# Kernel tuning notes

Measured on AMD Instinct MI355X. Metric: run time of the kernel, lower is better.

Reference implementation:

```python
import jax, jax.numpy as jnp
import numpy as np

# Module hyperparameters (init_kwargs)
OSFREQ = 8.0
MAXFREQ = 1.0
SP = 1.0
THRESH = 0.0

B, C, T = 8, 64, 1200


def _periodogram_cfg(n_samples):
    # Mirrors hypercoil's _periodogram_cfg
    timespan = SP * (n_samples + 1) - 1
    all_samples = np.arange(SP, timespan + 1, SP)
    freqstep = 1.0 / (timespan * OSFREQ)
    angular_frequencies = 2.0 * np.pi * np.arange(
        freqstep, MAXFREQ * n_samples / (2.0 * timespan) + freqstep, freqstep
    )
    return (
        jnp.asarray(angular_frequencies, jnp.float32),  # [K]
        jnp.asarray(all_samples, jnp.float32),          # [T]
    )


def setup_inputs() -> dict:
    key = jax.random.key(0)
    k1, k2 = jax.random.split(key)
    data = jax.random.normal(k1, (B, C, T), dtype=jnp.float32)
    mask = jax.random.randint(k2, (B, T), 0, 2).astype(bool)
    return {"input": data, "mask": mask}


def _fit_spectrum(basis, m, dm):
    # basis: [B,K,T] shifted trig basis; m: [B,T] mask weights; dm: [B,C,T] masked data
    num = jnp.einsum('bkt,bct->bkc', basis, dm)              # masked projection
    denom = jnp.einsum('bkt,bkt,bt->bk', basis, basis, m)    # masked basis norm
    coef = num / denom[..., None]
    if THRESH > 0:
        a = jnp.abs(coef)
        coef = jnp.where(a / a.max() > THRESH, coef, 0.0)
    return coef


def spectral_interpolate(data, mask):
    omega, t = _periodogram_cfg(data.shape[-1])  # [K], [T]
    m = mask.astype(data.dtype)                  # [B,T]
    arg2 = 2.0 * omega[:, None] * t[None, :]     # [K,T]
    # Lomb-Scargle time offsets tau per (batch, frequency), over observed samples only
    tau = jnp.arctan2(
        jnp.einsum('bt,kt->bk', m, jnp.sin(arg2)),
        jnp.einsum('bt,kt->bk', m, jnp.cos(arg2)),
    ) / (2.0 * omega)[None, :]                   # [B,K]
    theta = omega[None, :, None] * (t[None, None, :] - tau[:, :, None])  # [B,K,T]
    cosb = jnp.cos(theta)
    sinb = jnp.sin(theta)
    dm = data * m[:, None, :]                    # masked (degraded) data [B,C,T]
    c_coef = _fit_spectrum(cosb, m, dm)          # [B,K,C]
    s_coef = _fit_spectrum(sinb, m, dm)
    recon = (jnp.einsum('bkt,bkc->bct', cosb, c_coef)
             + jnp.einsum('bkt,bkc->bct', sinb, s_coef))      # [B,C,T]
    # Normalise: match std of reconstruction to std of observed data
    std_recon = jnp.std(recon, axis=-1, ddof=1, keepdims=True)
    cnt = m.sum(-1)[:, None, None]
    mu = dm.sum(-1, keepdims=True) / cnt
    var = ((data - mu) ** 2 * m[:, None, :]).sum(-1, keepdims=True) / (cnt - 1.0)
    std_orig = jnp.sqrt(var)
    recon = recon * (std_orig / std_recon)
    # Keep observed samples; fill censored samples with reconstruction
    return jnp.where(mask[:, None, :], data, recon)


def reference(input, mask):
    return spectral_interpolate(input, mask)
```

## Files before the change

### kernel.cpp

```cpp
#include <hip/hip_runtime.h>
#include <math.h>

#define B_ 8
#define C_ 64
#define M_ 512
#define T_ 1200
#define TP2 1280
#define KP 4864
#define K2P 9728
#define SPLITK 8
#define KCH 1216
#define NST1 20
#define NST2 19
#define TCH 152

#ifndef M_PI
#define M_PI 3.14159265358979323846
#endif

typedef _Float16 h8 __attribute__((ext_vector_type(8)));
typedef float f32x16 __attribute__((ext_vector_type(16)));
union H8 { h8 h; float4 v; _Float16 e[8]; };
union HP { _Float16 hh[2]; unsigned u; };
union F4U { float4 v; float f[4]; };

#define Z16v {0.f,0.f,0.f,0.f,0.f,0.f,0.f,0.f,0.f,0.f,0.f,0.f,0.f,0.f,0.f,0.f}
#define MFMA32(a, b, c) __builtin_amdgcn_mfma_f32_32x32x16_f16(a, b, c, 0, 0, 0)

__device__ __forceinline__ float2 cmul(float2 a, float2 b) {
    return make_float2(a.x * b.x - a.y * b.y, a.y * b.x + a.x * b.y);
}

__device__ __forceinline__ void gload16(const void* g, void* l) {
    __builtin_amdgcn_global_load_lds(
        (const __attribute__((address_space(1))) unsigned int*)g,
        (__attribute__((address_space(3))) unsigned int*)l, 16, 0, 0);
}

__device__ int detect_mode(const void* mask_raw) {
    __shared__ int sb0, sb1;
    if (threadIdx.x == 0) { sb0 = 0; sb1 = 0; }
    __syncthreads();
    const unsigned* wi = (const unsigned*)mask_raw;
    const float* wf = (const float*)mask_raw;
    int nw = (B_ * T_) >> 2;
    int badI = 0, badF = 0;
    for (int i = threadIdx.x; i < nw; i += blockDim.x) {
        unsigned v = wi[i];
        badI |= (v > 1u);
        float f = wf[i];
        badF |= !(f == 0.0f || f == 1.0f);
    }
    if (badI) sb0 = 1;
    if (badF) sb1 = 1;
    __syncthreads();
    return (!sb0) ? 0 : ((!sb1) ? 1 : 2);
}

__device__ __forceinline__ float mval(const void* mask_raw, int mode, int idx) {
    if (mode == 0) return (float)((const int*)mask_raw)[idx];
    if (mode == 1) return ((const float*)mask_raw)[idx];
    return (float)((const unsigned char*)mask_raw)[idx];
}

__global__ __launch_bounds__(256) void seed_kernel(
    const void* __restrict__ mask, float* __restrict__ mf, float* __restrict__ cnt,
    float2* __restrict__ rot1, float2* __restrict__ rot8,
    float2* __restrict__ rot32, float2* __restrict__ rot64,
    float2* __restrict__ rot2, float2* __restrict__ rot304, double fstep) {
    int bx = blockIdx.x, tid = threadIdx.x;
    if (bx < 114) {
        int tb = bx / 19;
        int k = (bx % 19) * 256 + tid;
        double om = 2.0 * M_PI * (fstep + (double)k * fstep);
        double w = (double)((float)om);
        double mult = (tb == 0) ? 1.0 : (tb == 1) ? 8.0 : (tb == 2) ? 32.0
                    : (tb == 3) ? 64.0 : (tb == 4) ? 2.0 : 304.0;
        double s, c;
        sincos(mult * w, &s, &c);
        float2 v = make_float2((float)c, (float)s);
        if (tb == 0)      rot1[k] = v;
        else if (tb == 1) rot8[k] = v;
        else if (tb == 2) rot32[k] = v;
        else if (tb == 3) rot64[k] = v;
        else if (tb == 4) rot2[k] = v;
        else              rot304[k] = v;
        return;
    }
    int mode = detect_mode(mask);
    if (bx < 124) {
        int i = ((bx - 114) * 256 + tid) * 4;
        if (i >= B_ * T_) return;
        F4U o;
        if (mode == 0) {
            int4 v = *(const int4*)((const int*)mask + i);
            o.f[0] = (float)v.x; o.f[1] = (float)v.y; o.f[2] = (float)v.z; o.f[3] = (float)v.w;
        } else if (mode == 1) {
            o.v = *(const float4*)((const float*)mask + i);
        } else {
            unsigned v = *(const unsigned*)((const unsigned char*)mask + i);
            o.f[0] = (float)(v & 0xff); o.f[1] = (float)((v >> 8) & 0xff);
            o.f[2] = (float)((v >> 16) & 0xff); o.f[3] = (float)((v >> 24) & 0xff);
        }
        *(float4*)&mf[i] = o.v;
        return;
    }
    {
        __shared__ float red[256];
        for (int b = 0; b < B_; b++) {
            float s = 0.f;
            for (int t = tid; t < T_; t += 256) s += mval(mask, mode, b * T_ + t);
            red[tid] = s; __syncthreads();
            for (int w = 128; w > 0; w >>= 1) {
                if (tid < w) red[tid] += red[tid + w];
                __syncthreads();
            }
            if (tid == 0) cnt[b] = red[0];
            __syncthreads();
        }
    }
}

__global__ __launch_bounds__(256) void prep2_kernel(
    const float* __restrict__ data, const float* __restrict__ mf,
    const float2* __restrict__ rot1t, const float2* __restrict__ rot8t,
    const float2* __restrict__ rot32t, const float2* __restrict__ rot64t,
    const float2* __restrict__ rot2t, const float2* __restrict__ rot304t,
    _Float16* __restrict__ dm, float* __restrict__ partS, float* __restrict__ partC,
    _Float16* __restrict__ Zb, _Float16* __restrict__ ZT, int K) {
    __shared__ float mfS[B_][TCH];
    __shared__ _Float16 sZ[128 * 80];
    __shared__ _Float16 sZT[64 * 136];
    int bx = blockIdx.x, tid = threadIdx.x;
    if (bx < 320) {
        int base = (bx * 256 + tid) * 8;
        int t = base % TP2, bc = base / TP2;
        H8 o;
        if (t < T_) {
            int b = bc >> 6;
            F4U d0, d1, m0, m1;
            d0.v = *(const float4*)&data[bc * T_ + t];
            d1.v = *(const float4*)&data[bc * T_ + t + 4];
            m0.v = *(const float4*)&mf[b * T_ + t];
            m1.v = *(const float4*)&mf[b * T_ + t + 4];
#pragma unroll
            for (int e = 0; e < 4; e++) {
                o.e[e]     = (_Float16)(d0.f[e] * m0.f[e]);
                o.e[e + 4] = (_Float16)(d1.f[e] * m1.f[e]);
            }
        } else {
#pragma unroll
            for (int e = 0; e < 8; e++) o.e[e] = (_Float16)0.f;
        }
        *(float4*)&dm[base] = o.v;
        return;
    }
    if (bx < 472) {
        int i0 = bx - 320;
        int kb = i0 % 19, chunk = i0 / 19;
        for (int i = tid; i < B_ * TCH; i += 256) {
            int b = i / TCH, tt = i % TCH;
            int t = chunk * TCH + tt;
            mfS[b][tt] = (t < T_) ? mf[b * T_ + t] : 0.f;
        }
        __syncthreads();
        int k = kb * 256 + tid;
        float2 r2 = rot2t[k];
        float2 r = r2;
        {
            int e = chunk;
            float2 p = rot304t[k];
            while (e) { if (e & 1) r = cmul(r, p); p = cmul(p, p); e >>= 1; }
        }
        float s2a[B_], c2a[B_];
#pragma unroll
        for (int b = 0; b < B_; b++) { s2a[b] = 0.f; c2a[b] = 0.f; }
        for (int tt = 0; tt < TCH; tt++) {
            float sv = r.y, cv = r.x;
#pragma unroll
            for (int b = 0; b < B_; b++) {
                float m = mfS[b][tt];
                s2a[b] = fmaf(m, sv, s2a[b]);
                c2a[b] = fmaf(m, cv, c2a[b]);
            }
            r = cmul(r, r2);
        }
#pragma unroll
        for (int b = 0; b < B_; b++) {
            partS[(size_t)(chunk * 8 + b) * KP + k] = s2a[b];
            partC[(size_t)(chunk * 8 + b) * KP + k] = c2a[b];
        }
        return;
    }
    {
        int i0 = bx - 472;
        int kb = i0 / 20, tb = i0 % 20;
        int k0 = kb * 64, t0 = tb * 64;
        int kk = tid >> 2, tq = tid & 3;
        int k = k0 + kk;
        float2 r1 = rot1t[k];
        float2 acc = r1;
        {
            float2 p = rot8t[k];
            if (tq & 1) acc = cmul(acc, p);
            p = cmul(p, p);
            if (tq & 2) acc = cmul(acc, p);
        }
        {
            int e = tb;
            float2 p = rot64t[k];
            while (e) { if (e & 1) acc = cmul(acc, p); p = cmul(p, p); e >>= 1; }
        }
        bool kv = (k < K);
        float2 r32 = rot32t[k];
#pragma unroll
        for (int j = 0; j < 2; j++) {
            float2 r = acc;
            H8 hc, hs;
#pragma unroll
            for (int d = 0; d < 8; d++) {
                int tl = tq * 8 + j * 32 + d;
                bool ok = kv && (t0 + tl < T_);
                float c = ok ? r.x : 0.f, s = ok ? r.y : 0.f;
                hc.e[d] = (_Float16)c; hs.e[d] = (_Float16)s;
                HP pk; pk.hh[0] = hc.e[d]; pk.hh[1] = hs.e[d];
                *(unsigned*)&sZT[tl * 136 + 2 * kk] = pk.u;
                r = cmul(r, r1);
            }
            int ch = tq + 4 * j;
            int rc = 2 * kk, rs = 2 * kk + 1;
            *(float4*)&sZ[rc * 80 + ((ch ^ (rc & 7)) << 3)] = hc.v;
            *(float4*)&sZ[rs * 80 + ((ch ^ (rs & 7)) << 3)] = hs.v;
            acc = cmul(acc, r32);
        }
        __syncthreads();
        {
            int c8 = tid & 7, rr = tid >> 3;
#pragma unroll
            for (int p = 0; p < 4; p++) {
                int row = p * 32 + rr;
                float4 v = *(const float4*)&sZ[row * 80 + ((c8 ^ (row & 7)) << 3)];
                *(float4*)&Zb[(size_t)(2 * k0 + row) * TP2 + t0 + c8 * 8] = v;
            }
        }
        {
            int c16 = tid & 15, rr = tid >> 4;
#pragma unroll
            for (int p = 0; p < 4; p++) {
                int row = p * 16 + rr;
                float4 v = *(const float4*)&sZT[row * 136 + c16 * 8];
                *(float4*)&ZT[(size_t)(t0 + row) * K2P + 2 * k0 + c16 * 8] = v;
            }
        }
    }
}

__global__ __launch_bounds__(256, 3) void gemm1x(
    const _Float16* __restrict__ dm, const _Float16* __restrict__ Zb,
    const float* __restrict__ partS, const float* __restrict__ partC,
    const float* __restrict__ cnt,
    _Float16* __restrict__ Wout) {
    __shared__ _Float16 lds[24576];
    char* ldsb = (char*)lds;
    int bx = blockIdx.x;
    int g = (bx & 7) * 76 + (bx >> 3);
    int mt = g & 7, nt = g >> 3;
    int m0 = mt * 64, n0 = nt * 128;
    int tid = threadIdx.x, lane = tid & 63, wv = tid >> 6;
    int ra = lane & 31, kg = lane >> 5, x = ra & 7;
    int wm = (wv & 1) * 32, wn = (wv >> 1) * 64;
    int r0 = wm + ra, q0 = wn + ra;
    f32x16 acc0 = Z16v, acc1 = Z16v;
    int sAo[2], sBo[4];
#pragma unroll
    for (int i = 0; i < 2; i++) {
        int g8 = i * 256 + tid;
        int r = g8 >> 3, c = g8 & 7;
        sAo[i] = r * 2560 + ((c ^ (r & 7)) << 4);
    }
#pragma unroll
    for (int i = 0; i < 4; i++) {
        int g8 = i * 256 + tid;
        int r = g8 >> 3, c = g8 & 7;
        sBo[i] = r * 2560 + ((c ^ (r & 7)) << 4);
    }
    const char* pA = (const char*)dm + (size_t)m0 * 2560;
    const char* pB = (const char*)Zb + (size_t)n0 * 2560;
#define STG1(BUFOFF, RC) do {                                                  \
        char* Ld_ = ldsb + (BUFOFF);                                           \
        _Pragma("unroll")                                                      \
        for (int i_ = 0; i_ < 2; i_++)                                         \
            gload16(pA + (RC) + sAo[i_], Ld_ + ((i_ * 256 + tid) << 4));       \
        _Pragma("unroll")                                                      \
        for (int i_ = 0; i_ < 4; i_++)                                         \
            gload16(pB + (RC) + sBo[i_], Ld_ + 8192 + ((i_ * 256 + tid) << 4));\
    } while (0)
    STG1(0, 0);
    __syncthreads();
    int cur = 0;
    for (int step = 0; step < NST1; step++) {
        if (step + 1 < NST1) STG1((cur ^ 1) * 24576, (step + 1) << 7);
        const char* LA = ldsb + cur * 24576;
        const char* LB = LA + 8192;
#pragma unroll
        for (int kc = 0; kc < 4; kc++) {
            int c = kc * 2 + kg;
            h8 a0 = *(const h8*)(LA + ((r0 * 8 + (c ^ x)) << 4));
            h8 b0 = *(const h8*)(LB + ((q0 * 8 + (c ^ x)) << 4));
            h8 b1 = *(const h8*)(LB + (((q0 + 32) * 8 + (c ^ x)) << 4));
            acc0 = MFMA32(a0, b0, acc0);
            acc1 = MFMA32(a0, b1, acc1);
        }
        __syncthreads();
        cur ^= 1;
    }
#undef STG1
    int bb = mt;
    int colk = lane & 31, rb4 = (lane >> 5) * 4;
    float cn = cnt[bb];
    float cpJ[2], spJ[2], rcJ[2], rsJ[2];
#pragma unroll
    for (int J = 0; J < 2; J++) {
        int k2 = n0 + wn + 32 * J + colk;
        int k = k2 >> 1;
        float s2 = 0.f, c2 = 0.f;
#pragma unroll
        for (int c = 0; c < 8; c++) {
            s2 += partS[(size_t)(c * 8 + bb) * KP + k];
            c2 += partC[(size_t)(c * 8 + bb) * KP + k];
        }
        float phi = 0.5f * atan2f(s2, c2);
        float cp = cosf(phi), sp = sinf(phi);
        float A = 0.5f * (cn + c2), D = 0.5f * (cn - c2), E = 0.5f * s2;
        cpJ[J] = cp; spJ[J] = sp;
        rcJ[J] = 1.f / (cp * cp * A + 2.f * cp * sp * E + sp * sp * D);
        rsJ[J] = 1.f / (sp * sp * A - 2.f * cp * sp * E + cp * cp * D);
    }
#define EPI1(ACC, J) {                                                         \
        int k2 = n0 + wn + 32 * (J) + colk;                                    \
        float cp = cpJ[J], sp = spJ[J];                                        \
        float rc_ = rcJ[J], rs_ = rsJ[J];                                      \
        int par = k2 & 1;                                                      \
        _Pragma("unroll")                                                      \
        for (int reg = 0; reg < 16; reg++) {                                   \
            float own = (ACC)[reg];                                            \
            float oth = __shfl_xor(own, 1);                                    \
            float p = par ? oth : own, q = par ? own : oth;                    \
            float cc = (cp * p + sp * q) * rc_;                                \
            float sc = (cp * q - sp * p) * rs_;                                \
            float val = par ? (sp * cc + cp * sc) : (cp * cc - sp * sc);       \
            int row = m0 + wm + rb4 + (reg & 3) + 8 * (reg >> 2);              \
            Wout[(size_t)row * K2P + k2] = (_Float16)val;                      \
        } }
    EPI1(acc0, 0); EPI1(acc1, 1);
#undef EPI1
}

__global__ __launch_bounds__(256, 3) void gemm2x(
    const _Float16* __restrict__ Wm, const _Float16* __restrict__ ZT,
    _Float16* __restrict__ rpart) {
    __shared__ _Float16 lds[24576];
    char* ldsb = (char*)lds;
    int bx = blockIdx.x;
    int sk = bx & 7;
    int g2 = bx >> 3;
    int mt = g2 & 3, tt = g2 >> 2;
    int m0 = mt * 128, t0 = tt * 64;
    int tid = threadIdx.x, lane = tid & 63, wv = tid >> 6;
    int ra = lane & 31, kg = lane >> 5, x = ra & 7;
    int wm = (wv & 1) * 64, wn = (wv >> 1) * 32;
    int r0 = wm + ra, q0 = wn + ra;
    f32x16 acc0 = Z16v, acc1 = Z16v;
    int sAo[4], sBo[2];
#pragma unroll
    for (int i = 0; i < 4; i++) {
        int g8 = i * 256 + tid;
        int r = g8 >> 3, c = g8 & 7;
        sAo[i] = r * 19456 + ((c ^ (r & 7)) << 4);
    }
#pragma unroll
    for (int i = 0; i < 2; i++) {
        int g8 = i * 256 + tid;
        int r = g8 >> 3, c = g8 & 7;
        sBo[i] = r * 19456 + ((c ^ (r & 7)) << 4);
    }
    const char* pA = (const char*)Wm + (size_t)m0 * 19456 + sk * 2432;
    const char* pB = (const char*)ZT + (size_t)t0 * 19456 + sk * 2432;
#define STG2(BUFOFF, RC) do {                                                  \
        char* Ld_ = ldsb + (BUFOFF);                                           \
        _Pragma("unroll")                                                      \
        for (int i_ = 0; i_ < 4; i_++)                                         \
            gload16(pA + (RC) + sAo[i_], Ld_ + ((i_ * 256 + tid) << 4));       \
        _Pragma("unroll")                                                      \
        for (int i_ = 0; i_ < 2; i_++)                                         \
            gload16(pB + (RC) + sBo[i_], Ld_ + 16384 + ((i_ * 256 + tid) << 4));\
    } while (0)
    STG2(0, 0);
    __syncthreads();
    int cur = 0;
    for (int step = 0; step < NST2; step++) {
        if (step + 1 < NST2) STG2((cur ^ 1) * 24576, (step + 1) << 7);
        const char* LA = ldsb + cur * 24576;
        const char* LB = LA + 16384;
#pragma unroll
        for (int kc = 0; kc < 4; kc++) {
            int c = kc * 2 + kg;
            h8 a0 = *(const h8*)(LA + ((r0 * 8 + (c ^ x)) << 4));
            h8 a1 = *(const h8*)(LA + (((r0 + 32) * 8 + (c ^ x)) << 4));
            h8 b0 = *(const h8*)(LB + ((q0 * 8 + (c ^ x)) << 4));
            acc0 = MFMA32(a0, b0, acc0);
            acc1 = MFMA32(a1, b0, acc1);
        }
        __syncthreads();
        cur ^= 1;
    }
#undef STG2
    int colk = lane & 31, rb4 = (lane >> 5) * 4;
    int t = t0 + wn + colk;
#define EPI2(ACC, I) {                                                         \
        _Pragma("unroll")                                                      \
        for (int reg = 0; reg < 16; reg++) {                                   \
            int row = m0 + wm + 32 * (I) + rb4 + (reg & 3) + 8 * (reg >> 2);   \
            rpart[(size_t)(sk * M_ + row) * TP2 + t] = (_Float16)(ACC)[reg];   \
        } }
    EPI2(acc0, 0); EPI2(acc1, 1);
#undef EPI2
}

__global__ __launch_bounds__(256) void norm3_kernel(
    const _Float16* __restrict__ rpart, const float* __restrict__ data,
    const float* __restrict__ mf, const float* __restrict__ cnt,
    float* __restrict__ out) {
    __shared__ float rsum[T_];
    __shared__ float4 red4[256];
    __shared__ float s_scale;
    int bc = blockIdx.x, b = bc >> 6;
    const size_t rbase = (size_t)bc * TP2;
    const size_t dbase = (size_t)bc * T_;
    const size_t rstr = (size_t)M_ * TP2;
    float sr = 0.f, srr = 0.f, sd = 0.f, sdd = 0.f;
    for (int t = threadIdx.x; t < T_; t += 256) {
        float r = 0.f;
#pragma unroll
        for (int s = 0; s < SPLITK; s++) r += (float)rpart[s * rstr + rbase + t];
        rsum[t] = r;
        float m = mf[b * T_ + t];
        float xv = data[dbase + t];
        sr += r; srr += r * r; sd += xv * m; sdd += xv * xv * m;
    }
    red4[threadIdx.x] = make_float4(sr, srr, sd, sdd);
    __syncthreads();
    for (int w = 128; w > 0; w >>= 1) {
        if (threadIdx.x < w) {
            float4 a = red4[threadIdx.x], c = red4[threadIdx.x + w];
            red4[threadIdx.x] = make_float4(a.x + c.x, a.y + c.y, a.z + c.z, a.w + c.w);
        }
        __syncthreads();
    }
    if (threadIdx.x == 0) {
        float4 v = red4[0];
        float cn = cnt[b];
        float varr = (v.y - v.x * v.x / (float)T_) / (float)(T_ - 1);
        float vard = (v.w - v.z * v.z / cn) / (cn - 1.f);
        s_scale = sqrtf(vard / varr);
    }
    __syncthreads();
    float scale = s_scale;
    for (int t = threadIdx.x; t < T_; t += 256) {
        float m = mf[b * T_ + t];
        out[dbase + t] = (m > 0.5f) ? data[dbase + t] : rsum[t] * scale;
    }
}

extern "C" void kernel_launch(void* const* d_in, const int* in_sizes, int n_in,
                              void* d_out, int out_size, void* d_ws, size_t ws_size,
                              hipStream_t stream) {
    const float* data = (const float*)d_in[0];
    const void* mask = d_in[1];
    float* out = (float*)d_out;

    const double timespan = 1.0 * (T_ + 1) - 1.0;
    const double fstep = 1.0 / (timespan * 8.0);
    const double stop = (1.0 * (double)T_) / (2.0 * timespan) + fstep;
    const int K = (int)ceil((stop - fstep) / fstep);

    char* w = (char*)d_ws;
    auto alloc = [&](size_t nbytes) {
        char* p = w;
        w += ((nbytes + 255) / 256) * 256;
        return p;
    };
    float*     mf    = (float*)    alloc((size_t)B_ * T_ * 4);
    float*     cnt   = (float*)    alloc(B_ * 4);
    float2*    rot1  = (float2*)   alloc((size_t)KP * 8);
    float2*    rot8  = (float2*)   alloc((size_t)KP * 8);
    float2*    rot32 = (float2*)   alloc((size_t)KP * 8);
    float2*    rot64 = (float2*)   alloc((size_t)KP * 8);
    float2*    rot2  = (float2*)   alloc((size_t)KP * 8);
    float2*    rot304= (float2*)   alloc((size_t)KP * 8);
    float*     partS = (float*)    alloc((size_t)64 * KP * 4);
    float*     partC = (float*)    alloc((size_t)64 * KP * 4);
    _Float16*  dm_h  = (_Float16*) alloc((size_t)M_ * TP2 * 2);
    _Float16*  Z     = (_Float16*) alloc((size_t)K2P * TP2 * 2);
    _Float16*  ZT    = (_Float16*) alloc((size_t)TP2 * K2P * 2);
    _Float16*  W     = (_Float16*) alloc((size_t)M_ * K2P * 2);
    _Float16*  rpart = (_Float16*) alloc((size_t)SPLITK * M_ * TP2 * 2);
    (void)ws_size; (void)in_sizes; (void)n_in; (void)out_size;

    seed_kernel<<<125, 256, 0, stream>>>(mask, mf, cnt, rot1, rot8, rot32,
                                         rot64, rot2, rot304, fstep);
    prep2_kernel<<<1992, 256, 0, stream>>>(data, mf, rot1, rot8, rot32, rot64,
                                           rot2, rot304, dm_h, partS, partC, Z, ZT, K);
    gemm1x<<<608, 256, 0, stream>>>(dm_h, Z, partS, partC, cnt, W);
    gemm2x<<<640, 256, 0, stream>>>(W, ZT, rpart);
    norm3_kernel<<<M_, 256, 0, stream>>>(rpart, data, mf, cnt, out);
}
```

Measured before the change: 88.52 us.

## Fuse seed and prep kernels, compute rotations inline and read mask directly

Merges the seed kernel into the prep kernel, dropping one launch and the intermediate rotation-table and float-mask buffers. Each block now computes its double-precision sincos rotation factors locally and reads the raw mask through mode detection, so the norm kernel also reads the mask directly. The cost is repeated double sincos work per block and a detect_mode scan of the whole mask in every block of prep and norm, which may outweigh the saved launch.

```diff
diff --git a/kernel.cpp b/kernel.cpp
--- a/kernel.cpp
+++ b/kernel.cpp
@@ -63,49 +63,158 @@
     return (float)((const unsigned char*)mask_raw)[idx];
 }
 
-__global__ __launch_bounds__(256) void seed_kernel(
-    const void* __restrict__ mask, float* __restrict__ mf, float* __restrict__ cnt,
-    float2* __restrict__ rot1, float2* __restrict__ rot8,
-    float2* __restrict__ rot32, float2* __restrict__ rot64,
-    float2* __restrict__ rot2, float2* __restrict__ rot304, double fstep) {
+__device__ __forceinline__ double omega_w(int k, double fstep) {
+    double om = 2.0 * M_PI * (fstep + (double)k * fstep);
+    return (double)((float)om);
+}
+
+__global__ __launch_bounds__(256) void prep3_kernel(
+    const float* __restrict__ data, const void* __restrict__ mask,
+    float* __restrict__ cnt,
+    _Float16* __restrict__ dm, float* __restrict__ partS, float* __restrict__ partC,
+    _Float16* __restrict__ Zb, _Float16* __restrict__ ZT, int K, double fstep) {
+    __shared__ float mfS[B_][TCH];
+    __shared__ _Float16 sZ[128 * 80];
+    __shared__ _Float16 sZT[64 * 136];
+    __shared__ float2 rotS[4][64];
     int bx = blockIdx.x, tid = threadIdx.x;
-    if (bx < 114) {
-        int tb = bx / 19;
-        int k = (bx % 19) * 256 + tid;
-        double om = 2.0 * M_PI * (fstep + (double)k * fstep);
-        double w = (double)((float)om);
-        double mult = (tb == 0) ? 1.0 : (tb == 1) ? 8.0 : (tb == 2) ? 32.0
-                    : (tb == 3) ? 64.0 : (tb == 4) ? 2.0 : 304.0;
-        double s, c;
-        sincos(mult * w, &s, &c);
-        float2 v = make_float2((float)c, (float)s);
-        if (tb == 0)      rot1[k] = v;
-        else if (tb == 1) rot8[k] = v;
-        else if (tb == 2) rot32[k] = v;
-        else if (tb == 3) rot64[k] = v;
-        else if (tb == 4) rot2[k] = v;
-        else              rot304[k] = v;
+    if (bx < 320) {
+        int mode = detect_mode(mask);
+        int base = (bx * 256 + tid) * 8;
+        int t = base % TP2, bc = base / TP2;
+        H8 o;
+        if (t < T_) {
+            int b = bc >> 6;
+            F4U d0, d1;
+            d0.v = *(const float4*)&data[bc * T_ + t];
+            d1.v = *(const float4*)&data[bc * T_ + t + 4];
+#pragma unroll
+            for (int e = 0; e < 4; e++) {
+                o.e[e]     = (_Float16)(d0.f[e] * mval(mask, mode, b * T_ + t + e));
+                o.e[e + 4] = (_Float16)(d1.f[e] * mval(mask, mode, b * T_ + t + 4 + e));
+            }
+        } else {
+#pragma unroll
+            for (int e = 0; e < 8; e++) o.e[e] = (_Float16)0.f;
+        }
+        *(float4*)&dm[base] = o.v;
         return;
     }
-    int mode = detect_mode(mask);
-    if (bx < 124) {
-        int i = ((bx - 114) * 256 + tid) * 4;
-        if (i >= B_ * T_) return;
-        F4U o;
-        if (mode == 0) {
-            int4 v = *(const int4*)((const int*)mask + i);
-            o.f[0] = (float)v.x; o.f[1] = (float)v.y; o.f[2] = (float)v.z; o.f[3] = (float)v.w;
-        } else if (mode == 1) {
-            o.v = *(const float4*)((const float*)mask + i);
-        } else {
-            unsigned v = *(const unsigned*)((const unsigned char*)mask + i);
-            o.f[0] = (float)(v & 0xff); o.f[1] = (float)((v >> 8) & 0xff);
-            o.f[2] = (float)((v >> 16) & 0xff); o.f[3] = (float)((v >> 24) & 0xff);
-        }
-        *(float4*)&mf[i] = o.v;
+    if (bx < 472) {
+        int mode = detect_mode(mask);
+        int i0 = bx - 320;
+        int kb = i0 % 19, chunk = i0 / 19;
+        for (int i = tid; i < B_ * TCH; i += 256) {
+            int b = i / TCH, tt = i % TCH;
+            int t = chunk * TCH + tt;
+            mfS[b][tt] = (t < T_) ? mval(mask, mode, b * T_ + t) : 0.f;
+        }
+        __syncthreads();
+        int k = kb * 256 + tid;
+        double w = omega_w(k, fstep);
+        double ds, dc;
+        sincos(2.0 * w, &ds, &dc);
+        float2 r2 = make_float2((float)dc, (float)ds);
+        sincos(304.0 * w, &ds, &dc);
+        float2 r304 = make_float2((float)dc, (float)ds);
+        float2 r = r2;
+        {
+            int e = chunk;
+            float2 p = r304;
+            while (e) { if (e & 1) r = cmul(r, p); p = cmul(p, p); e >>= 1; }
+        }
+        float s2a[B_], c2a[B_];
+#pragma unroll
+        for (int b = 0; b < B_; b++) { s2a[b] = 0.f; c2a[b] = 0.f; }
+        for (int tt = 0; tt < TCH; tt++) {
+            float sv = r.y, cv = r.x;
+#pragma unroll
+            for (int b = 0; b < B_; b++) {
+                float m = mfS[b][tt];
+                s2a[b] = fmaf(m, sv, s2a[b]);
+                c2a[b] = fmaf(m, cv, c2a[b]);
+            }
+            r = cmul(r, r2);
+        }
+#pragma unroll
+        for (int b = 0; b < B_; b++) {
+            partS[(size_t)(chunk * 8 + b) * KP + k] = s2a[b];
+            partC[(size_t)(chunk * 8 + b) * KP + k] = c2a[b];
+        }
         return;
     }
+    if (bx < 1992) {
+        int i0 = bx - 472;
+        int kb = i0 / 20, tb = i0 % 20;
+        int k0 = kb * 64, t0 = tb * 64;
+        int kk = tid >> 2, tq = tid & 3;
+        {
+            double w = omega_w(k0 + kk, fstep);
+            double mult = (tq == 0) ? 1.0 : (tq == 1) ? 8.0 : (tq == 2) ? 32.0 : 64.0;
+            double ds, dc;
+            sincos(mult * w, &ds, &dc);
+            rotS[tq][kk] = make_float2((float)dc, (float)ds);
+        }
+        __syncthreads();
+        int k = k0 + kk;
+        float2 r1 = rotS[0][kk];
+        float2 acc = r1;
+        {
+            float2 p = rotS[1][kk];
+            if (tq & 1) acc = cmul(acc, p);
+            p = cmul(p, p);
+            if (tq & 2) acc = cmul(acc, p);
+        }
+        {
+            int e = tb;
+            float2 p = rotS[3][kk];
+            while (e) { if (e & 1) acc = cmul(acc, p); p = cmul(p, p); e >>= 1; }
+        }
+        bool kv = (k < K);
+        float2 r32 = rotS[2][kk];
+#pragma unroll
+        for (int j = 0; j < 2; j++) {
+            float2 r = acc;
+            H8 hc, hs;
+#pragma unroll
+            for (int d = 0; d < 8; d++) {
+                int tl = tq * 8 + j * 32 + d;
+                bool ok = kv && (t0 + tl < T_);
+                float c = ok ? r.x : 0.f, s = ok ? r.y : 0.f;
+                hc.e[d] = (_Float16)c; hs.e[d] = (_Float16)s;
+                HP pk; pk.hh[0] = hc.e[d]; pk.hh[1] = hs.e[d];
+                *(unsigned*)&sZT[tl * 136 + 2 * kk] = pk.u;
+                r = cmul(r, r1);
+            }
+            int ch = tq + 4 * j;
+            int rc = 2 * kk, rs = 2 * kk + 1;
+            *(float4*)&sZ[rc * 80 + ((ch ^ (rc & 7)) << 3)] = hc.v;
+            *(float4*)&sZ[rs * 80 + ((ch ^ (rs & 7)) << 3)] = hs.v;
+            acc = cmul(acc, r32);
+        }
+        __syncthreads();
+        {
+            int c8 = tid & 7, rr = tid >> 3;
+#pragma unroll
+            for (int p = 0; p < 4; p++) {
+                int row = p * 32 + rr;
+                float4 v = *(const float4*)&sZ[row * 80 + ((c8 ^ (row & 7)) << 3)];
+                *(float4*)&Zb[(size_t)(2 * k0 + row) * TP2 + t0 + c8 * 8] = v;
+            }
+        }
+        {
+            int c16 = tid & 15, rr = tid >> 4;
+#pragma unroll
+            for (int p = 0; p < 4; p++) {
+                int row = p * 16 + rr;
+                float4 v = *(const float4*)&sZT[row * 136 + c16 * 8];
+                *(float4*)&ZT[(size_t)(t0 + row) * K2P + 2 * k0 + c16 * 8] = v;
+            }
+        }
+        return;
+    }
     {
+        int mode = detect_mode(mask);
         __shared__ float red[256];
         for (int b = 0; b < B_; b++) {
             float s = 0.f;
@@ -117,140 +226,6 @@
             }
             if (tid == 0) cnt[b] = red[0];
             __syncthreads();
-        }
-    }
-}
-
-__global__ __launch_bounds__(256) void prep2_kernel(
-    const float* __restrict__ data, const float* __restrict__ mf,
-    const float2* __restrict__ rot1t, const float2* __restrict__ rot8t,
-    const float2* __restrict__ rot32t, const float2* __restrict__ rot64t,
-    const float2* __restrict__ rot2t, const float2* __restrict__ rot304t,
-    _Float16* __restrict__ dm, float* __restrict__ partS, float* __restrict__ partC,
-    _Float16* __restrict__ Zb, _Float16* __restrict__ ZT, int K) {
-    __shared__ float mfS[B_][TCH];
-    __shared__ _Float16 sZ[128 * 80];
-    __shared__ _Float16 sZT[64 * 136];
-    int bx = blockIdx.x, tid = threadIdx.x;
-    if (bx < 320) {
-        int base = (bx * 256 + tid) * 8;
-        int t = base % TP2, bc = base / TP2;
-        H8 o;
-        if (t < T_) {
-            int b = bc >> 6;
-            F4U d0, d1, m0, m1;
-            d0.v = *(const float4*)&data[bc * T_ + t];
-            d1.v = *(const float4*)&data[bc * T_ + t + 4];
-            m0.v = *(const float4*)&mf[b * T_ + t];
-            m1.v = *(const float4*)&mf[b * T_ + t + 4];
-#pragma unroll
-            for (int e = 0; e < 4; e++) {
-                o.e[e]     = (_Float16)(d0.f[e] * m0.f[e]);
-                o.e[e + 4] = (_Float16)(d1.f[e] * m1.f[e]);
-            }
-        } else {
-#pragma unroll
-            for (int e = 0; e < 8; e++) o.e[e] = (_Float16)0.f;
-        }
-        *(float4*)&dm[base] = o.v;
-        return;
-    }
-    if (bx < 472) {
-        int i0 = bx - 320;
-        int kb = i0 % 19, chunk = i0 / 19;
-        for (int i = tid; i < B_ * TCH; i += 256) {
-            int b = i / TCH, tt = i % TCH;
-            int t = chunk * TCH + tt;
-            mfS[b][tt] = (t < T_) ? mf[b * T_ + t] : 0.f;
-        }
-        __syncthreads();
-        int k = kb * 256 + tid;
-        float2 r2 = rot2t[k];
-        float2 r = r2;
-        {
-            int e = chunk;
-            float2 p = rot304t[k];
-            while (e) { if (e & 1) r = cmul(r, p); p = cmul(p, p); e >>= 1; }
-        }
-        float s2a[B_], c2a[B_];
-#pragma unroll
-        for (int b = 0; b < B_; b++) { s2a[b] = 0.f; c2a[b] = 0.f; }
-        for (int tt = 0; tt < TCH; tt++) {
-            float sv = r.y, cv = r.x;
-#pragma unroll
-            for (int b = 0; b < B_; b++) {
-                float m = mfS[b][tt];
-                s2a[b] = fmaf(m, sv, s2a[b]);
-                c2a[b] = fmaf(m, cv, c2a[b]);
-            }
-            r = cmul(r, r2);
-        }
-#pragma unroll
-        for (int b = 0; b < B_; b++) {
-            partS[(size_t)(chunk * 8 + b) * KP + k] = s2a[b];
-            partC[(size_t)(chunk * 8 + b) * KP + k] = c2a[b];
-        }
-        return;
-    }
-    {
-        int i0 = bx - 472;
-        int kb = i0 / 20, tb = i0 % 20;
-        int k0 = kb * 64, t0 = tb * 64;
-        int kk = tid >> 2, tq = tid & 3;
-        int k = k0 + kk;
-        float2 r1 = rot1t[k];
-        float2 acc = r1;
-        {
-            float2 p = rot8t[k];
-            if (tq & 1) acc = cmul(acc, p);
-            p = cmul(p, p);
-            if (tq & 2) acc = cmul(acc, p);
-        }
-        {
-            int e = tb;
-            float2 p = rot64t[k];
-            while (e) { if (e & 1) acc = cmul(acc, p); p = cmul(p, p); e >>= 1; }
-        }
-        bool kv = (k < K);
-        float2 r32 = rot32t[k];
-#pragma unroll
-        for (int j = 0; j < 2; j++) {
-            float2 r = acc;
-            H8 hc, hs;
-#pragma unroll
-            for (int d = 0; d < 8; d++) {
-                int tl = tq * 8 + j * 32 + d;
-                bool ok = kv && (t0 + tl < T_);
-                float c = ok ? r.x : 0.f, s = ok ? r.y : 0.f;
-                hc.e[d] = (_Float16)c; hs.e[d] = (_Float16)s;
-                HP pk; pk.hh[0] = hc.e[d]; pk.hh[1] = hs.e[d];
-                *(unsigned*)&sZT[tl * 136 + 2 * kk] = pk.u;
-                r = cmul(r, r1);
-            }
-            int ch = tq + 4 * j;
-            int rc = 2 * kk, rs = 2 * kk + 1;
-            *(float4*)&sZ[rc * 80 + ((ch ^ (rc & 7)) << 3)] = hc.v;
-            *(float4*)&sZ[rs * 80 + ((ch ^ (rs & 7)) << 3)] = hs.v;
-            acc = cmul(acc, r32);
-        }
-        __syncthreads();
-        {
-            int c8 = tid & 7, rr = tid >> 3;
-#pragma unroll
-            for (int p = 0; p < 4; p++) {
-                int row = p * 32 + rr;
-                float4 v = *(const float4*)&sZ[row * 80 + ((c8 ^ (row & 7)) << 3)];
-                *(float4*)&Zb[(size_t)(2 * k0 + row) * TP2 + t0 + c8 * 8] = v;
-            }
-        }
-        {
-            int c16 = tid & 15, rr = tid >> 4;
-#pragma unroll
-            for (int p = 0; p < 4; p++) {
-                int row = p * 16 + rr;
-                float4 v = *(const float4*)&sZT[row * 136 + c16 * 8];
-                *(float4*)&ZT[(size_t)(t0 + row) * K2P + 2 * k0 + c16 * 8] = v;
-            }
         }
     }
 }
@@ -429,8 +404,9 @@
 
 __global__ __launch_bounds__(256) void norm3_kernel(
     const _Float16* __restrict__ rpart, const float* __restrict__ data,
-    const float* __restrict__ mf, const float* __restrict__ cnt,
+    const void* __restrict__ mask, const float* __restrict__ cnt,
     float* __restrict__ out) {
+    int mode = detect_mode(mask);
     __shared__ float rsum[T_];
     __shared__ float4 red4[256];
     __shared__ float s_scale;
@@ -444,7 +420,7 @@
 #pragma unroll
         for (int s = 0; s < SPLITK; s++) r += (float)rpart[s * rstr + rbase + t];
         rsum[t] = r;
-        float m = mf[b * T_ + t];
+        float m = mval(mask, mode, b * T_ + t);
         float xv = data[dbase + t];
         sr += r; srr += r * r; sd += xv * m; sdd += xv * xv * m;
     }
@@ -467,7 +443,7 @@
     __syncthreads();
     float scale = s_scale;
     for (int t = threadIdx.x; t < T_; t += 256) {
-        float m = mf[b * T_ + t];
+        float m = mval(mask, mode, b * T_ + t);
         out[dbase + t] = (m > 0.5f) ? data[dbase + t] : rsum[t] * scale;
     }
 }
@@ -490,14 +466,7 @@
         w += ((nbytes + 255) / 256) * 256;
         return p;
     };
-    float*     mf    = (float*)    alloc((size_t)B_ * T_ * 4);
     float*     cnt   = (float*)    alloc(B_ * 4);
-    float2*    rot1  = (float2*)   alloc((size_t)KP * 8);
-    float2*    rot8  = (float2*)   alloc((size_t)KP * 8);
-    float2*    rot32 = (float2*)   alloc((size_t)KP * 8);
-    float2*    rot64 = (float2*)   alloc((size_t)KP * 8);
-    float2*    rot2  = (float2*)   alloc((size_t)KP * 8);
-    float2*    rot304= (float2*)   alloc((size_t)KP * 8);
     float*     partS = (float*)    alloc((size_t)64 * KP * 4);
     float*     partC = (float*)    alloc((size_t)64 * KP * 4);
     _Float16*  dm_h  = (_Float16*) alloc((size_t)M_ * TP2 * 2);
@@ -507,11 +476,9 @@
     _Float16*  rpart = (_Float16*) alloc((size_t)SPLITK * M_ * TP2 * 2);
     (void)ws_size; (void)in_sizes; (void)n_in; (void)out_size;
 
-    seed_kernel<<<125, 256, 0, stream>>>(mask, mf, cnt, rot1, rot8, rot32,
-                                         rot64, rot2, rot304, fstep);
-    prep2_kernel<<<1992, 256, 0, stream>>>(data, mf, rot1, rot8, rot32, rot64,
-                                           rot2, rot304, dm_h, partS, partC, Z, ZT, K);
+    prep3_kernel<<<1993, 256, 0, stream>>>(data, mask, cnt, dm_h, partS, partC,
+                                           Z, ZT, K, fstep);
     gemm1x<<<608, 256, 0, stream>>>(dm_h, Z, partS, partC, cnt, W);
     gemm2x<<<640, 256, 0, stream>>>(W, ZT, rpart);
-    norm3_kernel<<<M_, 256, 0, stream>>>(rpart, data, mf, cnt, out);
-}
+    norm3_kernel<<<M_, 256, 0, stream>>>(rpart, data, mask, cnt, out);
+}
```

Measured after the change: 90.91 us. 1.03x slower.
